# Kernel tuning notes

Measured on AMD Instinct MI355X. Metric: run time of the kernel, lower is better.

Reference implementation:

```python
import jax, jax.numpy as jnp
import numpy as np

HIDDEN = 768
TMPL = 128  # template tokens stripped from x/xi
LN_EPS = 1e-5


def _layernorm(h, gamma, beta):
    mu = jnp.mean(h, axis=-1, keepdims=True)
    var = jnp.mean((h - mu) ** 2, axis=-1, keepdims=True)
    return (h - mu) * jax.lax.rsqrt(var + LN_EPS) * gamma + beta


def setup_inputs() -> dict:
    key = jax.random.key(0)
    ks = jax.random.split(key, 7)
    B, NT, LX, C = 32, 320, 704, HIDDEN
    s = C ** -0.5  # scale params so activations stay O(1)
    return {
        "T": jax.random.normal(ks[0], (B, NT, C), jnp.float32),
        "x": jax.random.normal(ks[1], (B, LX, C), jnp.float32),
        "xi": jax.random.normal(ks[2], (B, LX, C), jnp.float32),
        "Wq": jax.random.normal(ks[3], (C, C), jnp.float32) * s,
        "Wk": jax.random.normal(ks[4], (C, C), jnp.float32) * s,
        "Wv": jax.random.normal(ks[5], (C, C), jnp.float32) * s,
        "Wout": jax.random.normal(ks[6], (C, C), jnp.float32) * s,
        "gamma": jnp.ones((C,), jnp.float32),
        "beta": jnp.zeros((C,), jnp.float32),
    }


def reference(T, x, xi, Wq, Wk, Wv, Wout, gamma, beta):
    scale = T.shape[-1] ** -0.5
    xs = x[:, TMPL:]    # [B, N, C]
    xis = xi[:, TMPL:]  # [B, N, C]

    q = jnp.einsum("btc,cd->btd", T, Wq)
    k = jnp.einsum("bnc,cd->bnd", xs, Wk)
    ki = jnp.einsum("bnc,cd->bnd", xis, Wk)
    v = jnp.einsum("bnc,cd->bnd", xs, Wv)
    vi = jnp.einsum("bnc,cd->bnd", xis, Wv)

    aw = jax.nn.softmax(jnp.einsum("btd,bnd->btn", q, k) * scale, axis=-1)   # [B,Nt,N]
    awi = jax.nn.softmax(jnp.einsum("btd,bnd->btn", q, ki) * scale, axis=-1)  # [B,Nt,N]

    D = aw - awi
    num_rows = jnp.float32(D.shape[1])
    ones_cnt = jnp.sum(D > 0, axis=1).astype(jnp.float32)   # [B,N]
    half_cnt = jnp.sum(D == 0, axis=1).astype(jnp.float32)  # [B,N]
    rgb_ratio = (ones_cnt / num_rows)[..., None]   # [B,N,1]
    eq_ratio = (half_cnt / num_rows)[..., None]    # [B,N,1]
    tir_ratio = 1.0 - rgb_ratio - eq_ratio

    x_s = v * (rgb_ratio + eq_ratio) + vi * (tir_ratio + eq_ratio)  # [B,N,C]

    x_out = jnp.einsum("btn,bnc->btc", aw, v) @ Wout
    xi_out = jnp.einsum("btn,bnc->btc", awi, vi) @ Wout
    T_new = _layernorm(T + x_out + xi_out, gamma, beta)
    return x_s, T_new
```

## Files before the change

### kernel.cpp

```cpp
#include <hip/hip_runtime.h>

#define BB   32
#define NT   320
#define LX   704
#define TMPL 128
#define NS   576
#define CC   768
#define NS2  1152
#define LN_EPS 1e-5f

typedef __attribute__((ext_vector_type(8))) short short8;
typedef __attribute__((ext_vector_type(4))) float f32x4;
typedef unsigned long long u64;

typedef __attribute__((address_space(3))) void as3_void;
typedef __attribute__((address_space(1))) void as1_void;
#define GLDS16(g, l) __builtin_amdgcn_global_load_lds((const as1_void*)(g), (as3_void*)(l), 16, 0, 0)

__device__ __forceinline__ unsigned short f2bf(float f) {
    union { float f; unsigned u; } v; v.f = f;
    unsigned r = v.u + 0x7FFFu + ((v.u >> 16) & 1u);
    return (unsigned short)(r >> 16);
}
__device__ __forceinline__ float bf2f(unsigned short h) {
    union { unsigned u; float f; } v; v.u = ((unsigned)h) << 16;
    return v.f;
}

__device__ __forceinline__ int xcd_swz(int orig, int nwg) {
    int cpx = nwg >> 3;
    return (orig & 7) * cpx + (orig >> 3);
}

__device__ __forceinline__ float block_sum256(float v) {
    __shared__ float sm[4];
    #pragma unroll
    for (int o = 32; o > 0; o >>= 1) v += __shfl_down(v, o, 64);
    __syncthreads();
    if ((threadIdx.x & 63) == 0) sm[threadIdx.x >> 6] = v;
    __syncthreads();
    return sm[0] + sm[1] + sm[2] + sm[3];
}
__device__ __forceinline__ float block_max256(float v) {
    __shared__ float sm[4];
    #pragma unroll
    for (int o = 32; o > 0; o >>= 1) v = fmaxf(v, __shfl_down(v, o, 64));
    __syncthreads();
    if ((threadIdx.x & 63) == 0) sm[threadIdx.x >> 6] = v;
    __syncthreads();
    return fmaxf(fmaxf(sm[0], sm[1]), fmaxf(sm[2], sm[3]));
}

template<bool F32OUT>
__device__ __forceinline__ void gemm64_core(const short* __restrict__ Ab,
                                            const short* __restrict__ Bb,
                                            void* __restrict__ Cb,
                                            int m0, int n0,
                                            int N, int K, float alpha)
{
    __shared__ short As[64 * 32];
    __shared__ short Bs[128 * 32];
    const int tid  = threadIdx.x;
    const int lane = tid & 63;
    const int w    = tid >> 6;
    const int wr   = (w >> 1) * 32;
    const int wc   = (w & 1) * 64;

    const int srow = tid >> 2;
    const int g    = ((tid & 3) ^ ((srow >> 1) & 3)) * 8;
    const short* gA  = Ab + (long)(m0 + srow) * K + g;
    const short* gB0 = Bb + (long)(n0 + srow) * K + g;
    const short* gB1 = gB0 + (long)64 * K;
    short* lA  = As + tid * 8;
    short* lB0 = Bs + tid * 8;
    short* lB1 = Bs + 2048 + tid * 8;

    const int fl = lane & 15;
    const int ch = lane >> 4;

    f32x4 acc[2][4] = {};

    for (int k0 = 0; k0 < K; k0 += 32) {
        GLDS16(gA  + k0, lA);
        GLDS16(gB0 + k0, lB0);
        GLDS16(gB1 + k0, lB1);
        __syncthreads();

        short8 af[2], bfv[4];
        #pragma unroll
        for (int mt = 0; mt < 2; ++mt) {
            int row = wr + mt * 16 + fl;
            af[mt] = *(const short8*)(As + row * 32 + ((ch ^ ((row >> 1) & 3)) * 8));
        }
        #pragma unroll
        for (int nt = 0; nt < 4; ++nt) {
            int row = wc + nt * 16 + fl;
            bfv[nt] = *(const short8*)(Bs + row * 32 + ((ch ^ ((row >> 1) & 3)) * 8));
        }
        #pragma unroll
        for (int mt = 0; mt < 2; ++mt)
            #pragma unroll
            for (int nt = 0; nt < 4; ++nt)
                acc[mt][nt] = __builtin_amdgcn_mfma_f32_16x16x32_bf16(
                    af[mt], bfv[nt], acc[mt][nt], 0, 0, 0);
        __syncthreads();
    }

    float* Cf = (float*)Cb;
    unsigned short* Ch = (unsigned short*)Cb;
    const int rq = (lane >> 4) * 4;
    #pragma unroll
    for (int mt = 0; mt < 2; ++mt) {
        #pragma unroll
        for (int r = 0; r < 4; ++r) {
            long ro = (long)(m0 + wr + mt * 16 + rq + r) * N + n0 + wc + fl;
            #pragma unroll
            for (int nt = 0; nt < 4; ++nt) {
                float val = acc[mt][nt][r] * alpha;
                if (F32OUT) Cf[ro + nt * 16] = val;
                else        Ch[ro + nt * 16] = f2bf(val);
            }
        }
    }
}

template<bool F32OUT>
__global__ __launch_bounds__(256) void gemm64x(
    const short* __restrict__ A, const short* __restrict__ Bt, void* __restrict__ C,
    int N, int K, long sA, long sB, long sC, float alpha, int ntx, int nty)
{
    const int wg  = xcd_swz(blockIdx.x, gridDim.x);
    const int per = ntx * nty;
    const int b   = wg / per;
    const int rem = wg - b * per;
    const int n0  = (rem % ntx) * 128;
    const int m0  = (rem / ntx) * 64;
    void* Cb = F32OUT ? (void*)((float*)C + (long)b * sC)
                      : (void*)((unsigned short*)C + (long)b * sC);
    gemm64_core<F32OUT>(A + (long)b * sA, Bt + (long)b * sB, Cb, m0, n0, N, K, alpha);
}

__device__ __forceinline__ void gemm128_acc(const short* __restrict__ Ab,
                                            const short* __restrict__ Bb,
                                            int K, f32x4 acc[4][4])
{
    __shared__ short As[128 * 32];
    __shared__ short Bs[128 * 32];
    const int tid  = threadIdx.x;
    const int lane = tid & 63;
    const int w    = tid >> 6;
    const int wr   = (w >> 1) * 64;
    const int wc   = (w & 1) * 64;

    const int srow = tid >> 2;
    const int g    = ((tid & 3) ^ ((srow >> 1) & 3)) * 8;
    const short* gA0 = Ab + (long)srow * K + g;
    const short* gA1 = gA0 + (long)64 * K;
    const short* gB0 = Bb + (long)srow * K + g;
    const short* gB1 = gB0 + (long)64 * K;
    short* lA0 = As + tid * 8;
    short* lA1 = As + 2048 + tid * 8;
    short* lB0 = Bs + tid * 8;
    short* lB1 = Bs + 2048 + tid * 8;

    const int fl = lane & 15;
    const int ch = lane >> 4;

    for (int k0 = 0; k0 < K; k0 += 32) {
        GLDS16(gA0 + k0, lA0);
        GLDS16(gA1 + k0, lA1);
        GLDS16(gB0 + k0, lB0);
        GLDS16(gB1 + k0, lB1);
        __syncthreads();

        short8 af[4], bfv[4];
        #pragma unroll
        for (int mt = 0; mt < 4; ++mt) {
            int row = wr + mt * 16 + fl;
            af[mt] = *(const short8*)(As + row * 32 + ((ch ^ ((row >> 1) & 3)) * 8));
        }
        #pragma unroll
        for (int nt = 0; nt < 4; ++nt) {
            int row = wc + nt * 16 + fl;
            bfv[nt] = *(const short8*)(Bs + row * 32 + ((ch ^ ((row >> 1) & 3)) * 8));
        }
        #pragma unroll
        for (int mt = 0; mt < 4; ++mt)
            #pragma unroll
            for (int nt = 0; nt < 4; ++nt)
                acc[mt][nt] = __builtin_amdgcn_mfma_f32_16x16x32_bf16(
                    af[mt], bfv[nt], acc[mt][nt], 0, 0, 0);
        __syncthreads();
    }
}

template<bool F32OUT>
__global__ __launch_bounds__(256, 4) void gemm128(
    const short* __restrict__ A, const short* __restrict__ Bt, void* __restrict__ C,
    int N, int K, int ntiles_n, float alpha)
{
    const int wg = xcd_swz(blockIdx.x, gridDim.x);
    const int n0 = (wg % ntiles_n) * 128;
    const int m0 = (wg / ntiles_n) * 128;
    f32x4 acc[4][4] = {};
    gemm128_acc(A + (long)m0 * K, Bt + (long)n0 * K, K, acc);

    const int tid = threadIdx.x, lane = tid & 63, w = tid >> 6;
    const int wr = (w >> 1) * 64, wc = (w & 1) * 64;
    const int fl = lane & 15, rq = (lane >> 4) * 4;
    float* Cf = (float*)C;
    unsigned short* Ch = (unsigned short*)C;
    #pragma unroll
    for (int mt = 0; mt < 4; ++mt) {
        #pragma unroll
        for (int r = 0; r < 4; ++r) {
            long ro = (long)(m0 + wr + mt * 16 + rq + r) * N + n0 + wc + fl;
            #pragma unroll
            for (int nt = 0; nt < 4; ++nt) {
                float val = acc[mt][nt][r] * alpha;
                if (F32OUT) Cf[ro + nt * 16] = val;
                else        Ch[ro + nt * 16] = f2bf(val);
            }
        }
    }
}

#define PKV_NT 12
__global__ __launch_bounds__(256, 4) void proj_kv(
    const short* __restrict__ X, const short* __restrict__ WkvT,
    unsigned short* __restrict__ kkb, unsigned short* __restrict__ vvb,
    unsigned short* __restrict__ vvT)
{
    const int wg = xcd_swz(blockIdx.x, gridDim.x);
    const int n0 = (wg % PKV_NT) * 128;
    const int m0 = (wg / PKV_NT) * 128;
    f32x4 acc[4][4] = {};
    gemm128_acc(X + (long)m0 * CC, WkvT + (long)n0 * CC, CC, acc);

    const int tid = threadIdx.x, lane = tid & 63, w = tid >> 6;
    const int wr = (w >> 1) * 64, wc = (w & 1) * 64;
    const int fl = lane & 15, rq = (lane >> 4) * 4;

    const bool isv = (n0 >= CC);
    unsigned short* base = isv ? vvb : kkb;
    const int j0 = (isv ? n0 - CC : n0) + wc + fl;

    #pragma unroll
    for (int mt = 0; mt < 4; ++mt) {
        const int row0 = m0 + wr + mt * 16 + rq;
        const int isxi = (row0 >= BB * NS) ? 1 : 0;
        const int r2   = row0 - isxi * (BB * NS);
        const int b    = r2 / NS;
        const int n    = r2 - b * NS;
        unsigned short* po = base + (long)b * NS2 * CC
                                  + (long)isxi * NS * CC
                                  + (long)n * CC + j0;
        #pragma unroll
        for (int r = 0; r < 4; ++r) {
            #pragma unroll
            for (int nt = 0; nt < 4; ++nt)
                po[(long)r * CC + nt * 16] = f2bf(acc[mt][nt][r]);
        }
        if (isv) {
            const long ng = (long)isxi * NS + n;
            #pragma unroll
            for (int nt = 0; nt < 4; ++nt) {
                ushort4 o;
                o.x = f2bf(acc[mt][nt][0]); o.y = f2bf(acc[mt][nt][1]);
                o.z = f2bf(acc[mt][nt][2]); o.w = f2bf(acc[mt][nt][3]);
                *(ushort4*)(vvT + ((long)b * CC + j0 + nt * 16) * NS2 + ng) = o;
            }
        }
    }
}

__global__ void conv_in(const float* __restrict__ T, const float* __restrict__ x,
                        const float* __restrict__ xi,
                        unsigned short* __restrict__ Tb, unsigned short* __restrict__ xsb,
                        unsigned short* __restrict__ xisb)
{
    const int which = blockIdx.y;
    long i4 = ((long)blockIdx.x * 256 + threadIdx.x) * 4;
    const float* src; unsigned short* dst; long total; int rows, off, rpb;
    if (which == 0) { src = T;  dst = Tb;   total = (long)BB * NT * CC; rows = NT; off = 0;    rpb = NT; }
    else if (which == 1) { src = x;  dst = xsb;  total = (long)BB * NS * CC; rows = LX; off = TMPL; rpb = NS; }
    else            { src = xi; dst = xisb; total = (long)BB * NS * CC; rows = LX; off = TMPL; rpb = NS; }
    if (i4 >= total) return;
    int c   = (int)(i4 % CC);
    long rw = i4 / CC;
    int t   = (int)(rw % rpb);
    int b   = (int)(rw / rpb);
    const float4 f = *(const float4*)(src + ((long)b * rows + off + t) * CC + c);
    ushort4 o;
    o.x = f2bf(f.x); o.y = f2bf(f.y); o.z = f2bf(f.z); o.w = f2bf(f.w);
    *(ushort4*)(dst + i4) = o;
}

__global__ void conv_wt4(const float* __restrict__ Wq, const float* __restrict__ Wk,
                         const float* __restrict__ Wv, const float* __restrict__ Wo,
                         unsigned short* __restrict__ WqT, unsigned short* __restrict__ WkT,
                         unsigned short* __restrict__ WvT, unsigned short* __restrict__ WoT)
{
    const float* W; unsigned short* WT;
    switch (blockIdx.z) {
        case 0: W = Wq; WT = WqT; break;
        case 1: W = Wk; WT = WkT; break;
        case 2: W = Wv; WT = WvT; break;
        default: W = Wo; WT = WoT; break;
    }
    __shared__ float tile[32][33];
    const int c0 = blockIdx.x * 32, r0 = blockIdx.y * 32;
    const int tx = threadIdx.x & 31, ty = threadIdx.x >> 5;
    #pragma unroll
    for (int i = 0; i < 4; ++i)
        tile[ty + 8 * i][tx] = W[(long)(r0 + ty + 8 * i) * CC + c0 + tx];
    __syncthreads();
    #pragma unroll
    for (int i = 0; i < 4; ++i)
        WT[(long)(c0 + ty + 8 * i) * CC + r0 + tx] = f2bf(tile[tx][ty + 8 * i]);
}

__global__ void softmax_pack(const float* __restrict__ P, unsigned short* __restrict__ Pb,
                             u64* __restrict__ posm, u64* __restrict__ eqm)
{
    const long r = blockIdx.x;
    const float* p = P + r * NS2;
    const int tid = threadIdx.x;

    float a0 = p[tid], a1 = p[tid + 256], a2 = (tid < 64) ? p[tid + 512] : -1e30f;
    float m1 = block_max256(fmaxf(fmaxf(a0, a1), a2));
    float e0 = __expf(a0 - m1), e1 = __expf(a1 - m1), e2 = (tid < 64) ? __expf(a2 - m1) : 0.f;
    float s1 = block_sum256(e0 + e1 + e2);
    float i1 = 1.f / s1;
    e0 *= i1; e1 *= i1; e2 *= i1;

    const float* q = p + NS;
    float b0 = q[tid], b1 = q[tid + 256], b2 = (tid < 64) ? q[tid + 512] : -1e30f;
    float m2 = block_max256(fmaxf(fmaxf(b0, b1), b2));
    float f0 = __expf(b0 - m2), f1 = __expf(b1 - m2), f2v = (tid < 64) ? __expf(b2 - m2) : 0.f;
    float s2 = block_sum256(f0 + f1 + f2v);
    float i2 = 1.f / s2;
    f0 *= i2; f1 *= i2; f2v *= i2;

    unsigned short* ob = Pb + r * NS2;
    ob[tid] = f2bf(e0); ob[tid + 256] = f2bf(e1);
    if (tid < 64) ob[tid + 512] = f2bf(e2);
    ob[NS + tid] = f2bf(f0); ob[NS + tid + 256] = f2bf(f1);
    if (tid < 64) ob[NS + tid + 512] = f2bf(f2v);

    u64* pm = posm + r * 9;
    u64* em = eqm  + r * 9;
    const int wv = tid >> 6;
    float d0 = e0 - f0, d1 = e1 - f1, d2 = e2 - f2v;
    u64 P0 = __ballot(d0 > 0.f), E0 = __ballot(d0 == 0.f);
    if ((tid & 63) == 0) { pm[wv] = P0; em[wv] = E0; }
    u64 P1 = __ballot(d1 > 0.f), E1 = __ballot(d1 == 0.f);
    if ((tid & 63) == 0) { pm[4 + wv] = P1; em[4 + wv] = E1; }
    u64 P2 = __ballot(tid < 64 && d2 > 0.f), E2 = __ballot(tid < 64 && d2 == 0.f);
    if (tid == 0) { pm[8] = P2; em[8] = E2; }
}

__global__ void xs_fused(const u64* __restrict__ posm, const u64* __restrict__ eqm,
                         const unsigned short* __restrict__ vvb, float* __restrict__ out)
{
    const int gid = blockIdx.x;
    const int b = gid / NS, n = gid - b * NS;
    const int tid = threadIdx.x;
    const int wsel = n >> 6, bit = n & 63;
    float ones = 0.f, eqc = 0.f;
    for (int t = tid; t < NT; t += 256) {
        long o = ((long)(b * NT + t)) * 9 + wsel;
        ones += (float)((posm[o] >> bit) & 1);
        eqc  += (float)((eqm[o]  >> bit) & 1);
    }
    ones = block_sum256(ones);
    eqc  = block_sum256(eqc);
    float rgb = ones * (1.f / NT), e = eqc * (1.f / NT);
    float c1 = rgb + e;
    float c2 = (1.f - rgb - e) + e;
    const unsigned* pv  = (const unsigned*)(vvb + ((long)b * NS2 + n) * CC);
    const unsigned* pvi = (const unsigned*)(vvb + ((long)b * NS2 + n + NS) * CC);
    float* po = out + ((long)b * NS + n) * CC;
    for (int idx = tid; idx < CC / 2; idx += 256) {
        unsigned a = pv[idx], bb = pvi[idx];
        float2 o2;
        o2.x = bf2f((unsigned short)(a & 0xFFFF)) * c1 + bf2f((unsigned short)(bb & 0xFFFF)) * c2;
        o2.y = bf2f((unsigned short)(a >> 16))    * c1 + bf2f((unsigned short)(bb >> 16))    * c2;
        *(float2*)(po + 2 * idx) = o2;
    }
}

__global__ void add_ln(const float* __restrict__ T, const float* __restrict__ S2,
                       const float* __restrict__ gamma, const float* __restrict__ beta,
                       float* __restrict__ out)
{
    const long r = blockIdx.x;
    const int tid = threadIdx.x;
    const float* tp = T  + r * CC;
    const float* sp = S2 + r * CC;
    float h[3];
    float sum = 0.f;
    #pragma unroll
    for (int i = 0; i < 3; ++i) {
        h[i] = tp[tid + 256 * i] + sp[tid + 256 * i];
        sum += h[i];
    }
    sum = block_sum256(sum);
    float mu = sum * (1.f / CC);
    float varp = 0.f;
    #pragma unroll
    for (int i = 0; i < 3; ++i) { float d = h[i] - mu; varp += d * d; }
    varp = block_sum256(varp);
    float inv = rsqrtf(varp * (1.f / CC) + LN_EPS);
    #pragma unroll
    for (int i = 0; i < 3; ++i) {
        int c = tid + 256 * i;
        out[r * CC + c] = (h[i] - mu) * inv * gamma[c] + beta[c];
    }
}

extern "C" void kernel_launch(void* const* d_in, const int* in_sizes, int n_in,
                              void* d_out, int out_size, void* d_ws, size_t ws_size,
                              hipStream_t stream) {
    const float* T     = (const float*)d_in[0];
    const float* x     = (const float*)d_in[1];
    const float* xi    = (const float*)d_in[2];
    const float* Wq    = (const float*)d_in[3];
    const float* Wk    = (const float*)d_in[4];
    const float* Wv    = (const float*)d_in[5];
    const float* Wout  = (const float*)d_in[6];
    const float* gamma = (const float*)d_in[7];
    const float* beta  = (const float*)d_in[8];
    float* out = (float*)d_out;

    const long B_T  = (long)BB * NT * CC * 2;
    const long B_KK = (long)BB * NS2 * CC * 2;
    const long B_WT = (long)CC * CC * 2;
    const long B_XS = (long)BB * NS * CC * 2;
    const long B_PB = (long)BB * NT * NS2 * 2;
    const long B_MK = (long)BB * NT * 9 * 8;

    char* cur = (char*)d_ws;
    unsigned short* Tb   = (unsigned short*)cur; cur += B_T;
    unsigned short* qb   = (unsigned short*)cur; cur += B_T;
    unsigned short* kkb  = (unsigned short*)cur; cur += B_KK;
    unsigned short* WqT  = (unsigned short*)cur; cur += B_WT;
    unsigned short* WkT  = (unsigned short*)cur; cur += B_WT;
    unsigned short* WvT  = (unsigned short*)cur; cur += B_WT;
    unsigned short* WoT  = (unsigned short*)cur; cur += B_WT;
    unsigned short* vvb  = (unsigned short*)cur; cur += B_KK;
    unsigned short* vvT  = (unsigned short*)cur; cur += B_KK;
    unsigned short* xsb  = (unsigned short*)cur;
    unsigned short* xisb = xsb + (long)BB * NS * CC;  cur += 2 * B_XS;
    unsigned short* Pb   = (unsigned short*)cur; cur += B_PB;
    u64* posm            = (u64*)cur; cur += B_MK;
    u64* eqm             = (u64*)cur; cur += B_MK;
    if ((size_t)(cur - (char*)d_ws) > ws_size) return;

    float* P  = (float*)xsb;
    unsigned short* Sb = Tb;
    float* S2 = (float*)vvb;

    const float scale = 1.0f / sqrtf((float)CC);
    dim3 blk(256);

    conv_in<<<dim3((BB * NS * CC) / 1024, 3), blk, 0, stream>>>(T, x, xi, Tb, xsb, xisb);
    conv_wt4<<<dim3(CC / 32, CC / 32, 4), blk, 0, stream>>>(Wq, Wk, Wv, Wout, WqT, WkT, WvT, WoT);

    proj_kv<<<dim3(((2 * CC) / 128) * ((2 * BB * NS) / 128)), blk, 0, stream>>>(
        (const short*)xsb, (const short*)WkT, kkb, vvb, vvT);

    gemm128<false><<<dim3((CC / 128) * ((BB * NT) / 128)), blk, 0, stream>>>(
        (const short*)Tb, (const short*)WqT, qb, CC, CC, CC / 128, 1.f);

    gemm64x<true><<<dim3(BB * (NS2 / 128) * (NT / 64)), blk, 0, stream>>>(
        (const short*)qb, (const short*)kkb, P, NS2, CC,
        (long)NT * CC, (long)NS2 * CC, (long)NT * NS2, scale, NS2 / 128, NT / 64);

    softmax_pack<<<BB * NT, blk, 0, stream>>>(P, Pb, posm, eqm);

    xs_fused<<<BB * NS, blk, 0, stream>>>(posm, eqm, vvb, out);

    gemm64x<false><<<dim3(BB * (CC / 128) * (NT / 64)), blk, 0, stream>>>(
        (const short*)Pb, (const short*)vvT, Sb, CC, NS2,
        (long)NT * NS2, (long)CC * NS2, (long)NT * CC, 1.f, CC / 128, NT / 64);

    gemm128<true><<<dim3((CC / 128) * ((BB * NT) / 128)), blk, 0, stream>>>(
        (const short*)Sb, (const short*)WoT, S2, CC, CC, CC / 128, 1.f);

    add_ln<<<BB * NT, blk, 0, stream>>>(T, S2, gamma, beta, out + (long)BB * NS * CC);
}
```

Before: 547.7 us.

## Stage proj_kv epilogue through LDS and use one wave per softmax row

The K/V projection epilogue now writes the accumulator tile into a padded shared-memory buffer, then emits coalesced 16-byte row stores and builds the transposed V copy from LDS columns instead of scattered per-element and ushort4 stores. Separately, softmax_pack is rewritten so each 64-lane wave handles a full row with shuffle-only reductions, removing block-level barriers and launching four rows per block. The costs are extra LDS traffic and synchronisation in the GEMM epilogue, and possible bank conflicts in the column gather for the transpose.

```diff
diff --git a/kernel.cpp b/kernel.cpp
--- a/kernel.cpp
+++ b/kernel.cpp
@@ -40,15 +40,6 @@
     if ((threadIdx.x & 63) == 0) sm[threadIdx.x >> 6] = v;
     __syncthreads();
     return sm[0] + sm[1] + sm[2] + sm[3];
-}
-__device__ __forceinline__ float block_max256(float v) {
-    __shared__ float sm[4];
-    #pragma unroll
-    for (int o = 32; o > 0; o >>= 1) v = fmaxf(v, __shfl_down(v, o, 64));
-    __syncthreads();
-    if ((threadIdx.x & 63) == 0) sm[threadIdx.x >> 6] = v;
-    __syncthreads();
-    return fmaxf(fmaxf(sm[0], sm[1]), fmaxf(sm[2], sm[3]));
 }
 
 template<bool F32OUT>
@@ -142,10 +133,11 @@
 
 __device__ __forceinline__ void gemm128_acc(const short* __restrict__ Ab,
                                             const short* __restrict__ Bb,
-                                            int K, f32x4 acc[4][4])
-{
-    __shared__ short As[128 * 32];
-    __shared__ short Bs[128 * 32];
+                                            int K, f32x4 acc[4][4],
+                                            short* smem)
+{
+    short* As = smem;
+    short* Bs = smem + 4096;
     const int tid  = threadIdx.x;
     const int lane = tid & 63;
     const int w    = tid >> 6;
@@ -199,11 +191,12 @@
     const short* __restrict__ A, const short* __restrict__ Bt, void* __restrict__ C,
     int N, int K, int ntiles_n, float alpha)
 {
+    __shared__ short smem[8192];
     const int wg = xcd_swz(blockIdx.x, gridDim.x);
     const int n0 = (wg % ntiles_n) * 128;
     const int m0 = (wg / ntiles_n) * 128;
     f32x4 acc[4][4] = {};
-    gemm128_acc(A + (long)m0 * K, Bt + (long)n0 * K, K, acc);
+    gemm128_acc(A + (long)m0 * K, Bt + (long)n0 * K, K, acc, smem);
 
     const int tid = threadIdx.x, lane = tid & 63, w = tid >> 6;
     const int wr = (w >> 1) * 64, wc = (w & 1) * 64;
@@ -231,46 +224,62 @@
     unsigned short* __restrict__ kkb, unsigned short* __restrict__ vvb,
     unsigned short* __restrict__ vvT)
 {
+    __shared__ short smem[64 * 136];
     const int wg = xcd_swz(blockIdx.x, gridDim.x);
     const int n0 = (wg % PKV_NT) * 128;
     const int m0 = (wg / PKV_NT) * 128;
     f32x4 acc[4][4] = {};
-    gemm128_acc(X + (long)m0 * CC, WkvT + (long)n0 * CC, CC, acc);
+    gemm128_acc(X + (long)m0 * CC, WkvT + (long)n0 * CC, CC, acc, smem);
 
     const int tid = threadIdx.x, lane = tid & 63, w = tid >> 6;
-    const int wr = (w >> 1) * 64, wc = (w & 1) * 64;
+    const int wc = (w & 1) * 64;
     const int fl = lane & 15, rq = (lane >> 4) * 4;
 
     const bool isv = (n0 >= CC);
-    unsigned short* base = isv ? vvb : kkb;
-    const int j0 = (isv ? n0 - CC : n0) + wc + fl;
-
-    #pragma unroll
-    for (int mt = 0; mt < 4; ++mt) {
-        const int row0 = m0 + wr + mt * 16 + rq;
+    unsigned short* cbase = isv ? vvb : kkb;
+    const int j0base = isv ? n0 - CC : n0;
+
+    #pragma unroll
+    for (int h = 0; h < 2; ++h) {
+        if ((w >> 1) == h) {
+            #pragma unroll
+            for (int mt = 0; mt < 4; ++mt)
+                #pragma unroll
+                for (int nt = 0; nt < 4; ++nt)
+                    #pragma unroll
+                    for (int r = 0; r < 4; ++r)
+                        smem[(mt * 16 + rq + r) * 136 + wc + nt * 16 + fl] =
+                            (short)f2bf(acc[mt][nt][r]);
+        }
+        __syncthreads();
+        const int row0 = m0 + h * 64;
         const int isxi = (row0 >= BB * NS) ? 1 : 0;
         const int r2   = row0 - isxi * (BB * NS);
         const int b    = r2 / NS;
-        const int n    = r2 - b * NS;
-        unsigned short* po = base + (long)b * NS2 * CC
-                                  + (long)isxi * NS * CC
-                                  + (long)n * CC + j0;
-        #pragma unroll
-        for (int r = 0; r < 4; ++r) {
+        const int nb   = r2 - b * NS;
+
+        unsigned short* dst = cbase + (long)b * NS2 * CC + (long)isxi * NS * CC
+                                    + (long)nb * CC + j0base;
+        const int rowl = tid >> 2, cch = tid & 3;
+        #pragma unroll
+        for (int i = 0; i < 4; ++i)
+            *(short8*)(dst + (long)rowl * CC + (cch + i * 4) * 8) =
+                *(const short8*)(smem + rowl * 136 + (cch + i * 4) * 8);
+
+        if (isv) {
+            const int c = tid >> 1, seg = (tid & 1) * 32;
+            unsigned short* dT = vvT + ((long)b * CC + j0base + c) * NS2
+                                     + (long)isxi * NS + nb + seg;
             #pragma unroll
-            for (int nt = 0; nt < 4; ++nt)
-                po[(long)r * CC + nt * 16] = f2bf(acc[mt][nt][r]);
-        }
-        if (isv) {
-            const long ng = (long)isxi * NS + n;
-            #pragma unroll
-            for (int nt = 0; nt < 4; ++nt) {
-                ushort4 o;
-                o.x = f2bf(acc[mt][nt][0]); o.y = f2bf(acc[mt][nt][1]);
-                o.z = f2bf(acc[mt][nt][2]); o.w = f2bf(acc[mt][nt][3]);
-                *(ushort4*)(vvT + ((long)b * CC + j0 + nt * 16) * NS2 + ng) = o;
+            for (int i = 0; i < 4; ++i) {
+                short8 v;
+                #pragma unroll
+                for (int e = 0; e < 8; ++e)
+                    ((short*)&v)[e] = smem[(seg + i * 8 + e) * 136 + c];
+                *(short8*)(dT + i * 8) = v;
             }
         }
+        __syncthreads();
     }
 }
 
@@ -320,44 +329,55 @@
         WT[(long)(c0 + ty + 8 * i) * CC + r0 + tx] = f2bf(tile[tx][ty + 8 * i]);
 }
 
-__global__ void softmax_pack(const float* __restrict__ P, unsigned short* __restrict__ Pb,
-                             u64* __restrict__ posm, u64* __restrict__ eqm)
-{
-    const long r = blockIdx.x;
+__global__ __launch_bounds__(256) void softmax_pack(
+    const float* __restrict__ P, unsigned short* __restrict__ Pb,
+    u64* __restrict__ posm, u64* __restrict__ eqm)
+{
+    const int wv = threadIdx.x >> 6;
+    const int lane = threadIdx.x & 63;
+    const long r = (long)blockIdx.x * 4 + wv;
     const float* p = P + r * NS2;
-    const int tid = threadIdx.x;
-
-    float a0 = p[tid], a1 = p[tid + 256], a2 = (tid < 64) ? p[tid + 512] : -1e30f;
-    float m1 = block_max256(fmaxf(fmaxf(a0, a1), a2));
-    float e0 = __expf(a0 - m1), e1 = __expf(a1 - m1), e2 = (tid < 64) ? __expf(a2 - m1) : 0.f;
-    float s1 = block_sum256(e0 + e1 + e2);
-    float i1 = 1.f / s1;
-    e0 *= i1; e1 *= i1; e2 *= i1;
-
-    const float* q = p + NS;
-    float b0 = q[tid], b1 = q[tid + 256], b2 = (tid < 64) ? q[tid + 512] : -1e30f;
-    float m2 = block_max256(fmaxf(fmaxf(b0, b1), b2));
-    float f0 = __expf(b0 - m2), f1 = __expf(b1 - m2), f2v = (tid < 64) ? __expf(b2 - m2) : 0.f;
-    float s2 = block_sum256(f0 + f1 + f2v);
-    float i2 = 1.f / s2;
-    f0 *= i2; f1 *= i2; f2v *= i2;
+
+    float a[9], bq[9];
+    #pragma unroll
+    for (int i = 0; i < 9; ++i) a[i]  = p[lane + 64 * i];
+    #pragma unroll
+    for (int i = 0; i < 9; ++i) bq[i] = p[NS + lane + 64 * i];
+
+    float m1 = a[0], m2 = bq[0];
+    #pragma unroll
+    for (int i = 1; i < 9; ++i) { m1 = fmaxf(m1, a[i]); m2 = fmaxf(m2, bq[i]); }
+    #pragma unroll
+    for (int o = 32; o > 0; o >>= 1) {
+        m1 = fmaxf(m1, __shfl_xor(m1, o, 64));
+        m2 = fmaxf(m2, __shfl_xor(m2, o, 64));
+    }
+    float s1 = 0.f, s2 = 0.f;
+    #pragma unroll
+    for (int i = 0; i < 9; ++i) {
+        a[i]  = __expf(a[i]  - m1); s1 += a[i];
+        bq[i] = __expf(bq[i] - m2); s2 += bq[i];
+    }
+    #pragma unroll
+    for (int o = 32; o > 0; o >>= 1) {
+        s1 += __shfl_xor(s1, o, 64);
+        s2 += __shfl_xor(s2, o, 64);
+    }
+    const float i1 = 1.f / s1, i2 = 1.f / s2;
 
     unsigned short* ob = Pb + r * NS2;
-    ob[tid] = f2bf(e0); ob[tid + 256] = f2bf(e1);
-    if (tid < 64) ob[tid + 512] = f2bf(e2);
-    ob[NS + tid] = f2bf(f0); ob[NS + tid + 256] = f2bf(f1);
-    if (tid < 64) ob[NS + tid + 512] = f2bf(f2v);
-
     u64* pm = posm + r * 9;
     u64* em = eqm  + r * 9;
-    const int wv = tid >> 6;
-    float d0 = e0 - f0, d1 = e1 - f1, d2 = e2 - f2v;
-    u64 P0 = __ballot(d0 > 0.f), E0 = __ballot(d0 == 0.f);
-    if ((tid & 63) == 0) { pm[wv] = P0; em[wv] = E0; }
-    u64 P1 = __ballot(d1 > 0.f), E1 = __ballot(d1 == 0.f);
-    if ((tid & 63) == 0) { pm[4 + wv] = P1; em[4 + wv] = E1; }
-    u64 P2 = __ballot(tid < 64 && d2 > 0.f), E2 = __ballot(tid < 64 && d2 == 0.f);
-    if (tid == 0) { pm[8] = P2; em[8] = E2; }
+    #pragma unroll
+    for (int i = 0; i < 9; ++i) {
+        float e = a[i] * i1, f = bq[i] * i2;
+        ob[lane + 64 * i]      = f2bf(e);
+        ob[NS + lane + 64 * i] = f2bf(f);
+        float d = e - f;
+        u64 PP = __ballot(d > 0.f);
+        u64 EE = __ballot(d == 0.f);
+        if (lane == 0) { pm[i] = PP; em[i] = EE; }
+    }
 }
 
 __global__ void xs_fused(const u64* __restrict__ posm, const u64* __restrict__ eqm,
@@ -477,7 +497,7 @@
         (const short*)qb, (const short*)kkb, P, NS2, CC,
         (long)NT * CC, (long)NS2 * CC, (long)NT * NS2, scale, NS2 / 128, NT / 64);
 
-    softmax_pack<<<BB * NT, blk, 0, stream>>>(P, Pb, posm, eqm);
+    softmax_pack<<<dim3((BB * NT) / 4), blk, 0, stream>>>(P, Pb, posm, eqm);
 
     xs_fused<<<BB * NS, blk, 0, stream>>>(posm, eqm, vvb, out);
 
```

Measured after the change: 534.4 us. 2.4% less time.
